# Performance work log

Hardware: AMD Instinct MI355X
Metric: run time of the kernel (lower is better)

The kernel has to match this reference:

```python
import jax, jax.numpy as jnp
import numpy as np

B, N, F, U = 4, 4096, 256, 128
NEG = -1.0e9


def setup_inputs() -> dict:
    key = jax.random.key(0)
    k1, k2, k3, k4, k5 = jax.random.split(key, 5)
    inputs = jax.random.normal(k1, (B, N, F), dtype=jnp.float32)
    # Glorot-normal-like scales
    w = jax.random.normal(k2, (F, U), dtype=jnp.float32) * np.sqrt(2.0 / (F + U)).astype(np.float32)
    ai = jax.random.normal(k3, (U, N), dtype=jnp.float32) * np.sqrt(2.0 / (U + N)).astype(np.float32)
    aj = jax.random.normal(k4, (U, N), dtype=jnp.float32) * np.sqrt(2.0 / (U + N)).astype(np.float32)
    a = (jax.random.uniform(k5, (N, N)) < 0.004).astype(jnp.float32)
    adj = jnp.maximum(a, a.T)
    return {"inputs": inputs, "w": w, "ai": ai, "aj": aj, "adj": adj}


def reference(inputs, w, ai, aj, adj):
    # f: [B, N, U]
    f = jnp.einsum('bnf,fu->bnu', inputs, w)
    # self_attn[b,i,j] = (f ai)[b,i,j]; other_attn = transpose([0,2,1]) of (f aj)
    self_attn = jnp.einsum('bnu,um->bnm', f, ai)          # [B, N, N]
    other_attn = jnp.einsum('bnu,um->bmn', f, aj)         # transposed [B, N, N]
    mask = adj + jnp.eye(N, dtype=adj.dtype)              # allow self + neighbors
    attn = self_attn + other_attn + NEG * (1.0 - mask)
    attn = jax.nn.softmax(attn, axis=1)                   # softmax over rows (axis=1)
    # out[b,j,u] = sum_i f[b,i,u] * attn[b,i,j]
    out = jnp.einsum('biu,bij->bju', f, attn)
    return jax.nn.relu(out), attn
```

## Files before the change

kernel.cpp:

```cpp
#include <hip/hip_runtime.h>
#include <hip/hip_bf16.h>

#define NN 4096
#define UU 128
#define BB 4
#define FF 256
#define MAXD 128
#define ZB 1024

typedef float fv4 __attribute__((ext_vector_type(4)));

__device__ __forceinline__ unsigned short f2bf(float x) {
    unsigned int u = __float_as_uint(x);
    unsigned int r = (u + 0x7fffu + ((u >> 16) & 1u)) >> 16;
    return (unsigned short)r;
}
__device__ __forceinline__ float bf2f(unsigned short h) {
    return __uint_as_float(((unsigned int)h) << 16);
}

template <int CTRL, int RMASK>
__device__ __forceinline__ float dpp_step(float x) {
    int ti = __builtin_amdgcn_update_dpp(0, __float_as_int(x), CTRL, RMASK, 0xf, true);
    return x + __int_as_float(ti);
}
__device__ __forceinline__ float wave_sum_dpp(float x) {
    x = dpp_step<0x111, 0xf>(x);
    x = dpp_step<0x112, 0xf>(x);
    x = dpp_step<0x114, 0xf>(x);
    x = dpp_step<0x118, 0xf>(x);
    x = dpp_step<0x142, 0xa>(x);
    x = dpp_step<0x143, 0xc>(x);
    return __int_as_float(__builtin_amdgcn_readlane(__float_as_int(x), 63));
}

__global__ __launch_bounds__(256) void stage1(const float* __restrict__ A,
                                              const float* __restrict__ Wm,
                                              const float* __restrict__ adj,
                                              const float* __restrict__ ai,
                                              const float* __restrict__ aj,
                                              unsigned short* __restrict__ F,
                                              unsigned short* __restrict__ csc,
                                              int* __restrict__ cnt,
                                              int* __restrict__ dblf,
                                              unsigned short* __restrict__ aiT,
                                              unsigned short* __restrict__ ajT) {
    __shared__ __align__(16) char smem[43008];
    int t = threadIdx.x;
    int bid = blockIdx.x;

    if (bid < 512) {
        float (*As)[36]  = (float(*)[36])smem;
        float (*Ws)[132] = (float(*)[132])(smem + 9216);
        int r0 = bid * 32;
        int cg = t & 31;
        int rg = t >> 5;
        float acc[4][4] = {};
        for (int kc = 0; kc < FF; kc += 64) {
            {
                int row = t >> 3;
                int kb = (t & 7) * 8;
                const float* ap = A + (size_t)(r0 + row) * FF + kc + kb;
                float4 v0 = *(const float4*)(ap);
                float4 v1 = *(const float4*)(ap + 4);
                As[kb + 0][row] = v0.x; As[kb + 1][row] = v0.y;
                As[kb + 2][row] = v0.z; As[kb + 3][row] = v0.w;
                As[kb + 4][row] = v1.x; As[kb + 5][row] = v1.y;
                As[kb + 6][row] = v1.z; As[kb + 7][row] = v1.w;
            }
#pragma unroll
            for (int q = 0; q < 8; q++) {
                int idx = q * 256 + t;
                int k = idx >> 5;
                int c4 = (idx & 31) * 4;
                *(float4*)&Ws[k][c4] = *(const float4*)(Wm + (size_t)(kc + k) * UU + c4);
            }
            __syncthreads();
#pragma unroll 8
            for (int kk = 0; kk < 64; kk++) {
                float4 a4 = *(const float4*)&As[kk][rg * 4];
                float4 w4 = *(const float4*)&Ws[kk][cg * 4];
                acc[0][0] += a4.x * w4.x; acc[0][1] += a4.x * w4.y; acc[0][2] += a4.x * w4.z; acc[0][3] += a4.x * w4.w;
                acc[1][0] += a4.y * w4.x; acc[1][1] += a4.y * w4.y; acc[1][2] += a4.y * w4.z; acc[1][3] += a4.y * w4.w;
                acc[2][0] += a4.z * w4.x; acc[2][1] += a4.z * w4.y; acc[2][2] += a4.z * w4.z; acc[2][3] += a4.z * w4.w;
                acc[3][0] += a4.w * w4.x; acc[3][1] += a4.w * w4.y; acc[3][2] += a4.w * w4.z; acc[3][3] += a4.w * w4.w;
            }
            __syncthreads();
        }
#pragma unroll
        for (int i = 0; i < 4; i++) {
            ushort4 h;
            h.x = f2bf(acc[i][0]); h.y = f2bf(acc[i][1]);
            h.z = f2bf(acc[i][2]); h.w = f2bf(acc[i][3]);
            *(ushort4*)(F + (size_t)(r0 + rg * 4 + i) * UU + cg * 4) = h;
        }
    } else if (bid < 4608) {
        unsigned short* tmp = (unsigned short*)smem;
        int* cd = (int*)(smem + 256);
        int j = bid - 512;
        if (t == 0) { cd[0] = 0; cd[1] = 0; }
        __syncthreads();
        const float4* row = (const float4*)(adj + (size_t)j * NN);
#pragma unroll
        for (int k = 0; k < 4; k++) {
            int q = t + k * 256;
            float4 v = row[q];
            int base = q * 4;
            float vals[4] = {v.x, v.y, v.z, v.w};
#pragma unroll
            for (int s = 0; s < 4; s++) {
                int i = base + s;
                bool nz = (vals[s] != 0.0f);
                if (i == j) { if (nz) cd[1] = 1; nz = true; }
                if (nz) {
                    int p = atomicAdd(&cd[0], 1);
                    if (p < MAXD) tmp[p] = (unsigned short)i;
                }
            }
        }
        __syncthreads();
        int M = cd[0] < MAXD ? cd[0] : MAXD;
        if (t < M) csc[(size_t)j * MAXD + t] = tmp[t];
        if (t == 0) { cnt[j] = M; dblf[j] = cd[1]; }
    } else {
        float (*tile)[33] = (float(*)[33])smem;
        int r = bid - 4608;
        int z = r >> 9;
        int rem = r & 511;
        int n0 = (rem >> 2) * 32;
        int u0 = (rem & 3) * 32;
        const float* src = z ? aj : ai;
        unsigned short* dst = z ? ajT : aiT;
        int tx = t & 31;
        int ty = t >> 5;
        for (int rr = 0; rr < 32; rr += 8)
            tile[ty + rr][tx] = src[(size_t)(u0 + ty + rr) * NN + n0 + tx];
        __syncthreads();
        for (int rr = 0; rr < 32; rr += 8)
            dst[(size_t)(n0 + ty + rr) * UU + u0 + tx] = f2bf(tile[tx][ty + rr]);
    }
}

__global__ __launch_bounds__(256) void gat_zc(const unsigned short* __restrict__ csc,
                                              const int* __restrict__ cnt,
                                              const int* __restrict__ dblf,
                                              const unsigned short* __restrict__ f,
                                              const unsigned short* __restrict__ aiT,
                                              const unsigned short* __restrict__ ajT,
                                              float* __restrict__ out,
                                              float* __restrict__ tmpex,
                                              float* __restrict__ attn) {
    int tid = threadIdx.x;
    if (blockIdx.x >= NN) {
        size_t base = (size_t)(blockIdx.x - NN) * ((size_t)BB * NN * NN / ZB);
        fv4* p = (fv4*)(attn + base) + tid;
        fv4 z = {0.f, 0.f, 0.f, 0.f};
#pragma unroll 8
        for (int q = 0; q < 64; q++)
            __builtin_nontemporal_store(z, p + q * 256);
        return;
    }

    __shared__ unsigned short sidx[MAXD];
    int j = blockIdx.x;
    int lane = tid & 63, b = tid >> 6;
    int M = cnt[j];
    int oneh = dblf[j];
    if (tid < MAXD) sidx[tid] = csc[(size_t)j * MAXD + tid];

    const unsigned short* fb = f + (size_t)b * NN * UU;
    float* te = tmpex + ((size_t)b * NN + j) * MAXD;
    ushort2 fjh = *(const ushort2*)(fb + (size_t)j * UU + 2 * lane);
    float fjx = bf2f(fjh.x), fjy = bf2f(fjh.y);

    if (oneh) {
        int g0 = csc[(size_t)j * MAXD + lane];
        int g1 = csc[(size_t)j * MAXD + lane + 64];
        if (lane < M)      te[lane]      = (g0 == j) ? 1.0f : 0.0f;
        if (lane + 64 < M) te[lane + 64] = (g1 == j) ? 1.0f : 0.0f;
        float2 o;
        o.x = fjx > 0.0f ? fjx : 0.0f;
        o.y = fjy > 0.0f ? fjy : 0.0f;
        *(float2*)(out + ((size_t)(b * NN + j)) * UU + 2 * lane) = o;
        return;
    }
    __syncthreads();

    ushort2 aih = *(const ushort2*)(aiT + (size_t)j * UU + 2 * lane);
    float aix = bf2f(aih.x), aiy = bf2f(aih.y);
    float denom = 0.0f, acc0 = 0.0f, acc1 = 0.0f;
    float keep0 = 0.0f, keep1 = 0.0f;

    int e = 0;
    for (; e + 2 <= M; e += 2) {
        int ia = sidx[e], ib2 = sidx[e + 1];
        ushort2 fha = *(const ushort2*)(fb + (size_t)ia * UU + 2 * lane);
        ushort2 aha = *(const ushort2*)(ajT + (size_t)ia * UU + 2 * lane);
        ushort2 fhb = *(const ushort2*)(fb + (size_t)ib2 * UU + 2 * lane);
        ushort2 ahb = *(const ushort2*)(ajT + (size_t)ib2 * UU + 2 * lane);
        float fax = bf2f(fha.x), fay = bf2f(fha.y);
        float fbx = bf2f(fhb.x), fby = bf2f(fhb.y);
        float pa = fax * aix + fay * aiy + fjx * bf2f(aha.x) + fjy * bf2f(aha.y);
        float pb = fbx * aix + fby * aiy + fjx * bf2f(ahb.x) + fjy * bf2f(ahb.y);
        float sa = wave_sum_dpp(pa);
        float sb = wave_sum_dpp(pb);
        float exa = __expf(sa);
        float exb = __expf(sb);
        denom += exa + exb;
        acc0 += exa * fax + exb * fbx;
        acc1 += exa * fay + exb * fby;
        if ((e & 63) == lane)       { if (e < 64)     keep0 = exa; else keep1 = exa; }
        if (((e + 1) & 63) == lane) { if (e + 1 < 64) keep0 = exb; else keep1 = exb; }
    }
    for (; e < M; e++) {
        int i = sidx[e];
        ushort2 fih = *(const ushort2*)(fb + (size_t)i * UU + 2 * lane);
        ushort2 ajh = *(const ushort2*)(ajT + (size_t)i * UU + 2 * lane);
        float fix = bf2f(fih.x), fiy = bf2f(fih.y);
        float p = fix * aix + fiy * aiy + fjx * bf2f(ajh.x) + fjy * bf2f(ajh.y);
        float ex = __expf(wave_sum_dpp(p));
        denom += ex;
        acc0 += ex * fix;
        acc1 += ex * fiy;
        if ((e & 63) == lane) { if (e < 64) keep0 = ex; else keep1 = ex; }
    }
    float inv = 1.0f / denom;

    float2 o;
    o.x = acc0 * inv; o.y = acc1 * inv;
    o.x = o.x > 0.0f ? o.x : 0.0f;
    o.y = o.y > 0.0f ? o.y : 0.0f;
    *(float2*)(out + ((size_t)(b * NN + j)) * UU + 2 * lane) = o;

    if (lane < M)      te[lane]      = keep0 * inv;
    if (lane + 64 < M) te[lane + 64] = keep1 * inv;
}

__global__ __launch_bounds__(256) void attn_scatter(const unsigned short* __restrict__ csc,
                                                    const int* __restrict__ cnt,
                                                    const float* __restrict__ tmpex,
                                                    float* __restrict__ attn) {
    int j = blockIdx.x, tid = threadIdx.x;
    int lane = tid & 63, b = tid >> 6;
    int M = cnt[j];
    const float* te = tmpex + ((size_t)b * NN + j) * MAXD;
    if (lane < M) {
        int i = csc[(size_t)j * MAXD + lane];
        __builtin_nontemporal_store(te[lane], &attn[((size_t)(b * NN + i)) * NN + j]);
    }
    if (lane + 64 < M) {
        int i = csc[(size_t)j * MAXD + lane + 64];
        __builtin_nontemporal_store(te[lane + 64], &attn[((size_t)(b * NN + i)) * NN + j]);
    }
}

extern "C" void kernel_launch(void* const* d_in, const int* in_sizes, int n_in,
                              void* d_out, int out_size, void* d_ws, size_t ws_size,
                              hipStream_t stream) {
    const float* inputs = (const float*)d_in[0];
    const float* w      = (const float*)d_in[1];
    const float* ai     = (const float*)d_in[2];
    const float* aj     = (const float*)d_in[3];
    const float* adj    = (const float*)d_in[4];

    float* out  = (float*)d_out;
    float* attn = out + (size_t)BB * NN * UU;

    unsigned short* f   = (unsigned short*)d_ws;
    unsigned short* aiT = f + (size_t)BB * NN * UU;
    unsigned short* ajT = aiT + (size_t)NN * UU;
    unsigned short* csc = ajT + (size_t)NN * UU;
    int* cnt  = (int*)(csc + (size_t)NN * MAXD);
    int* dblf = cnt + NN;
    float* tmpex = (float*)(dblf + NN);

    stage1<<<5632, 256, 0, stream>>>(inputs, w, adj, ai, aj, f, csc, cnt, dblf, aiT, ajT);
    gat_zc<<<NN + ZB, 256, 0, stream>>>(csc, cnt, dblf, f, aiT, ajT, out, tmpex, attn);
    attn_scatter<<<NN, 256, 0, stream>>>(csc, cnt, tmpex, attn);
}
```

Measured before the change: 408.3 us.

## Fuse attention scatter into main kernel with mask-aware zero fill

The zero-fill blocks now skip the nonzero positions of each row, using the symmetric adjacency CSC lists, so the main blocks can write attention values straight into attn without a race. This removes the tmpex staging buffer and the separate scatter kernel launch. In exchange the zero-fill path reads each row's neighbor list, does a per-thread mask build over up to 128 entries, and uses scalar stores for chunks that contain neighbors. Correctness depends on the adjacency being symmetric so that column lists match row lists.

After: 889.5 us. +117.9%, slower.

```diff
diff --git a/kernel.cpp b/kernel.cpp
--- a/kernel.cpp
+++ b/kernel.cpp
@@ -148,16 +148,39 @@
                                               const unsigned short* __restrict__ aiT,
                                               const unsigned short* __restrict__ ajT,
                                               float* __restrict__ out,
-                                              float* __restrict__ tmpex,
                                               float* __restrict__ attn) {
     int tid = threadIdx.x;
+
     if (blockIdx.x >= NN) {
-        size_t base = (size_t)(blockIdx.x - NN) * ((size_t)BB * NN * NN / ZB);
-        fv4* p = (fv4*)(attn + base) + tid;
-        fv4 z = {0.f, 0.f, 0.f, 0.f};
-#pragma unroll 8
-        for (int q = 0; q < 64; q++)
-            __builtin_nontemporal_store(z, p + q * 256);
+        __shared__ unsigned short nb[MAXD];
+        __shared__ int mM;
+        int base_row = (blockIdx.x - NN) * 16;
+        for (int rr = 0; rr < 16; rr++) {
+            int r = base_row + rr;
+            int i = r & (NN - 1);
+            if (tid == 0) mM = cnt[i];
+            if (tid < MAXD) nb[tid] = csc[(size_t)i * MAXD + tid];
+            __syncthreads();
+            int M = mM;
+            unsigned mask = 0;
+            for (int s = 0; s < M; s++) {
+                int c = nb[s];
+                if ((c >> 4) == tid) mask |= 1u << (c & 15);
+            }
+            float* rowp = attn + (size_t)r * NN + 16 * tid;
+            if (mask == 0) {
+                fv4 z = {0.f, 0.f, 0.f, 0.f};
+#pragma unroll
+                for (int q = 0; q < 4; q++)
+                    __builtin_nontemporal_store(z, (fv4*)(rowp + 4 * q));
+            } else {
+#pragma unroll
+                for (int c = 0; c < 16; c++)
+                    if (!(mask & (1u << c)))
+                        __builtin_nontemporal_store(0.0f, rowp + c);
+            }
+            __syncthreads();
+        }
         return;
     }
 
@@ -169,15 +192,16 @@
     if (tid < MAXD) sidx[tid] = csc[(size_t)j * MAXD + tid];
 
     const unsigned short* fb = f + (size_t)b * NN * UU;
-    float* te = tmpex + ((size_t)b * NN + j) * MAXD;
     ushort2 fjh = *(const ushort2*)(fb + (size_t)j * UU + 2 * lane);
     float fjx = bf2f(fjh.x), fjy = bf2f(fjh.y);
 
     if (oneh) {
         int g0 = csc[(size_t)j * MAXD + lane];
         int g1 = csc[(size_t)j * MAXD + lane + 64];
-        if (lane < M)      te[lane]      = (g0 == j) ? 1.0f : 0.0f;
-        if (lane + 64 < M) te[lane + 64] = (g1 == j) ? 1.0f : 0.0f;
+        if (lane < M)
+            attn[((size_t)(b * NN + g0)) * NN + j] = (g0 == j) ? 1.0f : 0.0f;
+        if (lane + 64 < M)
+            attn[((size_t)(b * NN + g1)) * NN + j] = (g1 == j) ? 1.0f : 0.0f;
         float2 o;
         o.x = fjx > 0.0f ? fjx : 0.0f;
         o.y = fjy > 0.0f ? fjy : 0.0f;
@@ -232,26 +256,10 @@
     o.y = o.y > 0.0f ? o.y : 0.0f;
     *(float2*)(out + ((size_t)(b * NN + j)) * UU + 2 * lane) = o;
 
-    if (lane < M)      te[lane]      = keep0 * inv;
-    if (lane + 64 < M) te[lane + 64] = keep1 * inv;
-}
-
-__global__ __launch_bounds__(256) void attn_scatter(const unsigned short* __restrict__ csc,
-                                                    const int* __restrict__ cnt,
-                                                    const float* __restrict__ tmpex,
-                                                    float* __restrict__ attn) {
-    int j = blockIdx.x, tid = threadIdx.x;
-    int lane = tid & 63, b = tid >> 6;
-    int M = cnt[j];
-    const float* te = tmpex + ((size_t)b * NN + j) * MAXD;
-    if (lane < M) {
-        int i = csc[(size_t)j * MAXD + lane];
-        __builtin_nontemporal_store(te[lane], &attn[((size_t)(b * NN + i)) * NN + j]);
-    }
-    if (lane + 64 < M) {
-        int i = csc[(size_t)j * MAXD + lane + 64];
-        __builtin_nontemporal_store(te[lane + 64], &attn[((size_t)(b * NN + i)) * NN + j]);
-    }
+    if (lane < M)
+        attn[((size_t)(b * NN + sidx[lane])) * NN + j] = keep0 * inv;
+    if (lane + 64 < M)
+        attn[((size_t)(b * NN + sidx[lane + 64])) * NN + j] = keep1 * inv;
 }
 
 extern "C" void kernel_launch(void* const* d_in, const int* in_sizes, int n_in,
@@ -272,9 +280,7 @@
     unsigned short* csc = ajT + (size_t)NN * UU;
     int* cnt  = (int*)(csc + (size_t)NN * MAXD);
     int* dblf = cnt + NN;
-    float* tmpex = (float*)(dblf + NN);
 
     stage1<<<5632, 256, 0, stream>>>(inputs, w, adj, ai, aj, f, csc, cnt, dblf, aiT, ajT);
-    gat_zc<<<NN + ZB, 256, 0, stream>>>(csc, cnt, dblf, f, aiT, ajT, out, tmpex, attn);
-    attn_scatter<<<NN, 256, 0, stream>>>(csc, cnt, tmpex, attn);
-}
+    gat_zc<<<NN + ZB, 256, 0, stream>>>(csc, cnt, dblf, f, aiT, ajT, out, attn);
+}
```
